# Performance work log

Measured on AMD Instinct MI355X. Metric: run time of the kernel, lower is better.

The kernel has to match this reference:

```python
import jax, jax.numpy as jnp
import numpy as np

CELU_ALPHA = 0.1  # torchani default
DIMS = [384, 160, 128, 96, 1]


def setup_inputs() -> dict:
    key = jax.random.key(0)
    ks = jax.random.split(key, 10)
    E, N, D = 4, 200000, DIMS[0]
    species = jax.random.randint(ks[0], (1, N), 0, E)
    aev = jax.random.normal(ks[1], (1, N, D), dtype=jnp.float32)
    params = {}
    for li in range(4):
        din, dout = DIMS[li], DIMS[li + 1]
        scale = 1.0 / np.sqrt(din)
        params[f"W{li+1}"] = jax.random.uniform(ks[2 + 2 * li], (E, din, dout), jnp.float32, -scale, scale)
        params[f"b{li+1}"] = jax.random.uniform(ks[3 + 2 * li], (E, dout), jnp.float32, -scale, scale)
    return dict(aev=aev, species=species, **params)


def _celu(x):
    return jax.nn.celu(x, alpha=CELU_ALPHA)


def reference(aev, species, W1, b1, W2, b2, W3, b3, W4, b4):
    # aev: [1, N, D] -> flatten(0,1) like the torch code; species: [1, N]
    x = aev.reshape(-1, aev.shape[-1])            # [N, D]
    sp = species.reshape(-1)                       # [N]
    E = W1.shape[0]
    # Run every expert MLP over all rows (jit-friendly equivalent of the
    # per-species index_select dispatch); mask-combine at the end.
    h = _celu(jnp.einsum('nd,edh->enh', x, W1) + b1[:, None, :])   # [E, N, 160]
    h = _celu(jnp.einsum('enh,ehk->enk', h, W2) + b2[:, None, :])  # [E, N, 128]
    h = _celu(jnp.einsum('enk,ekm->enm', h, W3) + b3[:, None, :])  # [E, N, 96]
    out = (jnp.einsum('enm,emo->eno', h, W4) + b4[:, None, :])[..., 0]  # [E, N]
    onehot = jax.nn.one_hot(sp, E, dtype=out.dtype)                # [N, E]
    # energy_list[i] = sum over atoms with species==i of net_i output
    energy_list = jnp.sum(out * onehot.T, axis=1)                  # [E]
    return jnp.sum(energy_list, keepdims=True)                     # [1]
```

## Files before the change

### kernel.cpp

```cpp
#include <hip/hip_runtime.h>
#include <hip/hip_bf16.h>
#include <stdint.h>

typedef __attribute__((ext_vector_type(8))) short bf16x8;
typedef __attribute__((ext_vector_type(4))) float f32x4;
#define MFMA16 __builtin_amdgcn_mfma_f32_16x16x32_bf16

__device__ __forceinline__ float celu_f(float x) {
    return x > 0.f ? x : 0.1f * (__expf(x * 10.f) - 1.f);
}
__device__ __forceinline__ uint16_t bfb(float x) {
    __hip_bfloat16 h = __float2bfloat16(x);
    return *reinterpret_cast<const uint16_t*>(&h);
}
__device__ __forceinline__ uint32_t pack2(float lo, float hi) {
    return (uint32_t)bfb(lo) | ((uint32_t)bfb(hi) << 16);
}
__device__ __forceinline__ bf16x8 cvt8(float4 a, float4 b) {
    bf16x8 r;
    r[0] = (short)bfb(a.x); r[1] = (short)bfb(a.y); r[2] = (short)bfb(a.z); r[3] = (short)bfb(a.w);
    r[4] = (short)bfb(b.x); r[5] = (short)bfb(b.y); r[6] = (short)bfb(b.z); r[7] = (short)bfb(b.w);
    return r;
}
__device__ __forceinline__ void gload16(const void* g, void* l) {
    __builtin_amdgcn_global_load_lds(
        (const __attribute__((address_space(1))) unsigned int*)g,
        (__attribute__((address_space(3))) unsigned int*)l, 16, 0, 0);
}

template <int DIN, int DOUT>
__global__ void wsplit_kernel(const float* __restrict__ W, __hip_bfloat16* __restrict__ out) {
    constexpr int MB = DOUT / 16, KB = DIN / 32;
    constexpr int PER_E = MB * KB * 512;
    const int idx = blockIdx.x * 256 + threadIdx.x;
    if (idx >= 4 * PER_E) return;
    const int e = idx / PER_E;
    int r = idx % PER_E;
    const int mb = r / (KB * 512); r %= KB * 512;
    const int kb = r / 512;        r %= 512;
    const int l = r / 8, j = r % 8;
    const int m = mb * 16 + (l % 16);
    const int k = kb * 32 + (l / 16) * 8 + j;
    const float w = W[((size_t)e * DIN + k) * DOUT + m];
    const __hip_bfloat16 hi = __float2bfloat16(w);
    const float lof = w - __bfloat162float(hi);
    const size_t base = (size_t)(idx / 8) * 16;
    out[base + j]     = hi;
    out[base + 8 + j] = __float2bfloat16(lof);
}

__global__ void bucket_kernel(const int* __restrict__ species, int N,
                              int* __restrict__ counts, int* __restrict__ bidx) {
    __shared__ int lcount[4];
    __shared__ int lbase[4];
    const int t = threadIdx.x;
    if (t < 4) lcount[t] = 0;
    __syncthreads();
    const int n = blockIdx.x * blockDim.x + t;
    int sp = 0, lo = 0;
    const bool valid = (n < N);
    if (valid) {
        sp = species[n];
        lo = atomicAdd(&lcount[sp], 1);
    }
    __syncthreads();
    if (t < 4) lbase[t] = atomicAdd(&counts[t], lcount[t]);
    __syncthreads();
    if (valid) bidx[sp * N + lbase[sp] + lo] = n;
}

__global__ void sched_kernel(const int* __restrict__ counts, int* __restrict__ tbase) {
    if (threadIdx.x == 0 && blockIdx.x == 0) {
        int tacc = 0;
        tbase[0] = 0;
        for (int e = 0; e < 4; ++e) { tacc += (counts[e] + 127) >> 7; tbase[e + 1] = tacc; }
    }
}

__device__ __forceinline__ void stage_for(int s, int e, int w, int l,
                                          const char* w1b, const char* w2b,
                                          const char* w3b, char* slot) {
    if (s >= 42) return;
    const int half = s & 1;
    if (s < 24) {
        const int kb = s >> 1;
        for (int u = w; u < 10; u += 4) {
            const int mb = half * 5 + (u >> 1), h = u & 1;
            const char* src = w1b + ((((size_t)e * 10 + mb) * 12 + kb) << 11) + l * 32 + h * 16;
            gload16(src, slot + u * 1024);
        }
    } else if (s < 34) {
        const int kb = (s - 24) >> 1;
        for (int u = w; u < 8; u += 4) {
            const int mb = half * 4 + (u >> 1), h = u & 1;
            const char* src = w2b + ((((size_t)e * 8 + mb) * 5 + kb) << 11) + l * 32 + h * 16;
            gload16(src, slot + u * 1024);
        }
    } else {
        const int kb = (s - 34) >> 1;
        for (int u = w; u < 6; u += 4) {
            const int mb = half * 3 + (u >> 1), h = u & 1;
            const char* src = w3b + ((((size_t)e * 6 + mb) * 4 + kb) << 11) + l * 32 + h * 16;
            gload16(src, slot + u * 1024);
        }
    }
}

template <int MBH>
__device__ __forceinline__ void consume_slot(const char* slot, int l,
                                             bf16x8 x0, bf16x8 x1, f32x4 (*acc)[2]) {
#pragma unroll
    for (int i = 0; i < MBH; ++i) {
        const bf16x8 whi = *(const bf16x8*)(slot + i * 2048 + l * 16);
        const bf16x8 wlo = *(const bf16x8*)(slot + i * 2048 + 1024 + l * 16);
        acc[i][0] = MFMA16(whi, x0, acc[i][0], 0, 0, 0);
        acc[i][0] = MFMA16(wlo, x0, acc[i][0], 0, 0, 0);
        acc[i][1] = MFMA16(whi, x1, acc[i][1], 0, 0, 0);
        acc[i][1] = MFMA16(wlo, x1, acc[i][1], 0, 0, 0);
    }
}

template <int MB>
__device__ __forceinline__ void pack_epi(const f32x4 (*acc)[2], const float* bb, int q,
                                         uint32_t (*pk)[2][2]) {
    const int fr = q * 4;
#pragma unroll
    for (int mb = 0; mb < MB; ++mb) {
        const float4 bl = *(const float4*)(bb + mb * 16 + fr);
        const float bv[4] = {bl.x, bl.y, bl.z, bl.w};
#pragma unroll
        for (int c = 0; c < 2; ++c) {
            const float o0 = celu_f(acc[mb][c][0] + bv[0]);
            const float o1 = celu_f(acc[mb][c][1] + bv[1]);
            const float o2 = celu_f(acc[mb][c][2] + bv[2]);
            const float o3 = celu_f(acc[mb][c][3] + bv[3]);
            pk[mb][c][0] = pack2(o0, o1);
            pk[mb][c][1] = pack2(o2, o3);
        }
    }
}

__device__ __forceinline__ bf16x8 xchg(uint32_t pe0, uint32_t pe1,
                                       uint32_t po0, uint32_t po1, int a, int q) {
    union { uint32_t u[4]; bf16x8 v; } r;
#pragma unroll
    for (int d = 0; d < 4; ++d) {
        const int src = a + 16 * ((2 * q + (d >> 1)) & 3);
        const uint32_t ve = __shfl((d & 1) ? pe1 : pe0, src);
        const uint32_t vo = __shfl((d & 1) ? po1 : po0, src);
        r.u[d] = (q >= 2) ? vo : ve;
    }
    return r.v;
}

__global__ __launch_bounds__(256, 3) void mlp_mfma_kernel(
    const float* __restrict__ aev, const int* __restrict__ bidx,
    const int* __restrict__ counts, const int* __restrict__ tbase, int N,
    const __hip_bfloat16* __restrict__ wsw1, const float* __restrict__ b1,
    const __hip_bfloat16* __restrict__ wsw2, const float* __restrict__ b2,
    const __hip_bfloat16* __restrict__ wsw3, const float* __restrict__ b3,
    const float* __restrict__ W4, const float* __restrict__ b4,
    float* __restrict__ partials) {
    __shared__ __align__(16) char Wslot[2][10240];
    const int b = blockIdx.x, t = threadIdx.x;
    const int tb1 = tbase[1], tb2 = tbase[2], tb3 = tbase[3], tb4 = tbase[4];
    if (b >= tb4) return;
    const int e = (b >= tb1) + (b >= tb2) + (b >= tb3);
    const int tile = b - (e == 0 ? 0 : e == 1 ? tb1 : e == 2 ? tb2 : tb3);
    const int cnt = counts[e];
    const int w = t >> 6, l = t & 63;
    const int wbase = tile * 128 + w * 32;
    const int a = l & 15, q = l >> 4;
    const int g0 = wbase + a, g1 = wbase + 16 + a;
    const bool v0g = g0 < cnt, v1g = g1 < cnt;
    const int i0 = bidx[e * N + min(g0, cnt - 1)];
    const int i1 = bidx[e * N + min(g1, cnt - 1)];
    const float* row0 = aev + (size_t)i0 * 384 + q * 8;
    const float* row1 = aev + (size_t)i1 * 384 + q * 8;

    const char* w1b = (const char*)wsw1;
    const char* w2b = (const char*)wsw2;
    const char* w3b = (const char*)wsw3;

    float4 na = *(const float4*)(row0);
    float4 nb = *(const float4*)(row0 + 4);
    float4 nc = *(const float4*)(row1);
    float4 nd = *(const float4*)(row1 + 4);
    stage_for(0, e, w, l, w1b, w2b, w3b, &Wslot[0][0]);
    __syncthreads();

    int step = 0;

    f32x4 acc1[10][2] = {};
#pragma unroll 1
    for (int kb = 0; kb < 12; ++kb) {
        const bf16x8 x0 = cvt8(na, nb), x1 = cvt8(nc, nd);
        stage_for(step + 1, e, w, l, w1b, w2b, w3b, &Wslot[(step + 1) & 1][0]);
        consume_slot<5>(&Wslot[step & 1][0], l, x0, x1, &acc1[0]);
        __syncthreads(); ++step;
        if (kb < 11) {
            na = *(const float4*)(row0 + (kb + 1) * 32);
            nb = *(const float4*)(row0 + (kb + 1) * 32 + 4);
            nc = *(const float4*)(row1 + (kb + 1) * 32);
            nd = *(const float4*)(row1 + (kb + 1) * 32 + 4);
        }
        stage_for(step + 1, e, w, l, w1b, w2b, w3b, &Wslot[(step + 1) & 1][0]);
        consume_slot<5>(&Wslot[step & 1][0], l, x0, x1, &acc1[5]);
        __syncthreads(); ++step;
    }

    uint32_t pk1[10][2][2];
    pack_epi<10>(acc1, b1 + e * 160, q, pk1);

    f32x4 acc2[8][2] = {};
#pragma unroll
    for (int kb2 = 0; kb2 < 5; ++kb2) {
        const bf16x8 h0 = xchg(pk1[2 * kb2][0][0], pk1[2 * kb2][0][1],
                               pk1[2 * kb2 + 1][0][0], pk1[2 * kb2 + 1][0][1], a, q);
        const bf16x8 h1 = xchg(pk1[2 * kb2][1][0], pk1[2 * kb2][1][1],
                               pk1[2 * kb2 + 1][1][0], pk1[2 * kb2 + 1][1][1], a, q);
        const int s0 = 24 + 2 * kb2;
        stage_for(s0 + 1, e, w, l, w1b, w2b, w3b, &Wslot[(s0 + 1) & 1][0]);
        consume_slot<4>(&Wslot[s0 & 1][0], l, h0, h1, &acc2[0]);
        __syncthreads();
        stage_for(s0 + 2, e, w, l, w1b, w2b, w3b, &Wslot[(s0 + 2) & 1][0]);
        consume_slot<4>(&Wslot[(s0 + 1) & 1][0], l, h0, h1, &acc2[4]);
        __syncthreads();
    }

    uint32_t pk2[8][2][2];
    pack_epi<8>(acc2, b2 + e * 128, q, pk2);

    f32x4 acc3[6][2] = {};
#pragma unroll
    for (int kb3 = 0; kb3 < 4; ++kb3) {
        const bf16x8 h0 = xchg(pk2[2 * kb3][0][0], pk2[2 * kb3][0][1],
                               pk2[2 * kb3 + 1][0][0], pk2[2 * kb3 + 1][0][1], a, q);
        const bf16x8 h1 = xchg(pk2[2 * kb3][1][0], pk2[2 * kb3][1][1],
                               pk2[2 * kb3 + 1][1][0], pk2[2 * kb3 + 1][1][1], a, q);
        const int s0 = 34 + 2 * kb3;
        stage_for(s0 + 1, e, w, l, w1b, w2b, w3b, &Wslot[(s0 + 1) & 1][0]);
        consume_slot<3>(&Wslot[s0 & 1][0], l, h0, h1, &acc3[0]);
        __syncthreads();
        stage_for(s0 + 2, e, w, l, w1b, w2b, w3b, &Wslot[(s0 + 2) & 1][0]);
        consume_slot<3>(&Wslot[(s0 + 1) & 1][0], l, h0, h1, &acc3[3]);
        __syncthreads();
    }

    const int fr = q * 4;
    float en0 = 0.f, en1 = 0.f;
#pragma unroll
    for (int mb = 0; mb < 6; ++mb) {
        const float4 bl = *(const float4*)(b3 + e * 96 + mb * 16 + fr);
        const float4 wv = *(const float4*)(W4 + e * 96 + mb * 16 + fr);
        const float bv[4] = {bl.x, bl.y, bl.z, bl.w};
        const float wb[4] = {wv.x, wv.y, wv.z, wv.w};
#pragma unroll
        for (int r = 0; r < 4; ++r) {
            en0 += celu_f(acc3[mb][0][r] + bv[r]) * wb[r];
            en1 += celu_f(acc3[mb][1][r] + bv[r]) * wb[r];
        }
    }
    en0 += __shfl_xor(en0, 16); en0 += __shfl_xor(en0, 32);
    en1 += __shfl_xor(en1, 16); en1 += __shfl_xor(en1, 32);
    const float b4e = b4[e];
    float p = 0.f;
    if (l < 16) p = (v0g ? en0 + b4e : 0.f) + (v1g ? en1 + b4e : 0.f);
#pragma unroll
    for (int off = 1; off <= 32; off <<= 1) p += __shfl_xor(p, off);
    if (l == 0) partials[b * 4 + w] = p;
}

__global__ void reduce_kernel(const float* __restrict__ partials,
                              const int* __restrict__ tbase, float* __restrict__ out) {
    __shared__ float wsum[4];
    const int n = tbase[4] * 4;
    const int t = threadIdx.x;
    float s = 0.f;
    for (int i = t; i < n; i += 256) s += partials[i];
#pragma unroll
    for (int off = 32; off; off >>= 1) s += __shfl_down(s, off);
    if ((t & 63) == 0) wsum[t >> 6] = s;
    __syncthreads();
    if (t == 0) out[0] = wsum[0] + wsum[1] + wsum[2] + wsum[3];
}

extern "C" void kernel_launch(void* const* d_in, const int* in_sizes, int n_in,
                              void* d_out, int out_size, void* d_ws, size_t ws_size,
                              hipStream_t stream) {
    const float* aev     = (const float*)d_in[0];
    const int*   species = (const int*)d_in[1];
    const float* W1 = (const float*)d_in[2];
    const float* b1 = (const float*)d_in[3];
    const float* W2 = (const float*)d_in[4];
    const float* b2 = (const float*)d_in[5];
    const float* W3 = (const float*)d_in[6];
    const float* b3 = (const float*)d_in[7];
    const float* W4 = (const float*)d_in[8];
    const float* b4 = (const float*)d_in[9];
    float* out = (float*)d_out;

    const int N = in_sizes[1];
    const int gridx_max = (N + 127) / 128 + 4;

    char* ws = (char*)d_ws;
    int* counts = (int*)ws;
    int* tbase  = (int*)(ws + 16);
    float* partials = (float*)(ws + 256);
    size_t off = 256 + (size_t)gridx_max * 4 * sizeof(float);
    off = (off + 255) & ~(size_t)255;
    __hip_bfloat16* wsw1 = (__hip_bfloat16*)(ws + off); off += (size_t)4 * 384 * 160 * 2 * 2;
    __hip_bfloat16* wsw2 = (__hip_bfloat16*)(ws + off); off += (size_t)4 * 160 * 128 * 2 * 2;
    __hip_bfloat16* wsw3 = (__hip_bfloat16*)(ws + off); off += (size_t)4 * 128 * 96 * 2 * 2;
    int* bidx = (int*)(ws + off);

    hipMemsetAsync(d_ws, 0, 16, stream);

    wsplit_kernel<384, 160><<<(4 * 384 * 160 + 255) / 256, 256, 0, stream>>>(W1, wsw1);
    wsplit_kernel<160, 128><<<(4 * 160 * 128 + 255) / 256, 256, 0, stream>>>(W2, wsw2);
    wsplit_kernel<128, 96><<<(4 * 128 * 96 + 255) / 256, 256, 0, stream>>>(W3, wsw3);

    bucket_kernel<<<(N + 255) / 256, 256, 0, stream>>>(species, N, counts, bidx);
    sched_kernel<<<1, 64, 0, stream>>>(counts, tbase);

    mlp_mfma_kernel<<<gridx_max, 256, 0, stream>>>(aev, bidx, counts, tbase, N,
                                                   wsw1, b1, wsw2, b2, wsw3, b3, W4, b4,
                                                   partials);

    reduce_kernel<<<1, 256, 0, stream>>>(partials, tbase, out);
}
```

Before: 175.6 us.

## Restructure MLP K-loop barriers to prefetch activations earlier and drop memset

Replaces __syncthreads with a custom vmcnt(0)+s_barrier placed before each stage/consume pair, so the LDS double buffer is synchronized at the top of each step rather than the end. Next-chunk activation loads are issued right after the barrier into separate registers, which gives them more time in flight. The separate hipMemsetAsync is removed and the counts buffer is zeroed inside the first wsplit kernel launch, saving one enqueue. This uses more registers for the prefetch copies and relies on the hand-placed waitcnt covering the global_load_lds traffic.

```diff
diff --git a/kernel.cpp b/kernel.cpp
--- a/kernel.cpp
+++ b/kernel.cpp
@@ -27,9 +27,16 @@
         (const __attribute__((address_space(1))) unsigned int*)g,
         (__attribute__((address_space(3))) unsigned int*)l, 16, 0, 0);
 }
+__device__ __forceinline__ void wait_barrier() {
+    asm volatile("s_waitcnt vmcnt(0)" ::: "memory");
+    asm volatile("s_barrier" ::: "memory");
+    __builtin_amdgcn_sched_barrier(0);
+}
 
 template <int DIN, int DOUT>
-__global__ void wsplit_kernel(const float* __restrict__ W, __hip_bfloat16* __restrict__ out) {
+__global__ void wsplit_kernel(const float* __restrict__ W, __hip_bfloat16* __restrict__ out,
+                              int* counts_zero) {
+    if (counts_zero && blockIdx.x == 0 && threadIdx.x < 4) counts_zero[threadIdx.x] = 0;
     constexpr int MB = DOUT / 16, KB = DIN / 32;
     constexpr int PER_E = MB * KB * 512;
     const int idx = blockIdx.x * 256 + threadIdx.x;
@@ -187,26 +194,25 @@
     float4 nc = *(const float4*)(row1);
     float4 nd = *(const float4*)(row1 + 4);
     stage_for(0, e, w, l, w1b, w2b, w3b, &Wslot[0][0]);
-    __syncthreads();
-
-    int step = 0;
 
     f32x4 acc1[10][2] = {};
+    float4 pa, pb, pc, pd;
 #pragma unroll 1
     for (int kb = 0; kb < 12; ++kb) {
+        wait_barrier();
+        if (kb < 11) {
+            pa = *(const float4*)(row0 + (kb + 1) * 32);
+            pb = *(const float4*)(row0 + (kb + 1) * 32 + 4);
+            pc = *(const float4*)(row1 + (kb + 1) * 32);
+            pd = *(const float4*)(row1 + (kb + 1) * 32 + 4);
+        }
         const bf16x8 x0 = cvt8(na, nb), x1 = cvt8(nc, nd);
-        stage_for(step + 1, e, w, l, w1b, w2b, w3b, &Wslot[(step + 1) & 1][0]);
-        consume_slot<5>(&Wslot[step & 1][0], l, x0, x1, &acc1[0]);
-        __syncthreads(); ++step;
-        if (kb < 11) {
-            na = *(const float4*)(row0 + (kb + 1) * 32);
-            nb = *(const float4*)(row0 + (kb + 1) * 32 + 4);
-            nc = *(const float4*)(row1 + (kb + 1) * 32);
-            nd = *(const float4*)(row1 + (kb + 1) * 32 + 4);
-        }
-        stage_for(step + 1, e, w, l, w1b, w2b, w3b, &Wslot[(step + 1) & 1][0]);
-        consume_slot<5>(&Wslot[step & 1][0], l, x0, x1, &acc1[5]);
-        __syncthreads(); ++step;
+        stage_for(2 * kb + 1, e, w, l, w1b, w2b, w3b, &Wslot[(2 * kb + 1) & 1][0]);
+        consume_slot<5>(&Wslot[(2 * kb) & 1][0], l, x0, x1, &acc1[0]);
+        wait_barrier();
+        stage_for(2 * kb + 2, e, w, l, w1b, w2b, w3b, &Wslot[(2 * kb + 2) & 1][0]);
+        consume_slot<5>(&Wslot[(2 * kb + 1) & 1][0], l, x0, x1, &acc1[5]);
+        na = pa; nb = pb; nc = pc; nd = pd;
     }
 
     uint32_t pk1[10][2][2];
@@ -220,12 +226,12 @@
         const bf16x8 h1 = xchg(pk1[2 * kb2][1][0], pk1[2 * kb2][1][1],
                                pk1[2 * kb2 + 1][1][0], pk1[2 * kb2 + 1][1][1], a, q);
         const int s0 = 24 + 2 * kb2;
+        wait_barrier();
         stage_for(s0 + 1, e, w, l, w1b, w2b, w3b, &Wslot[(s0 + 1) & 1][0]);
         consume_slot<4>(&Wslot[s0 & 1][0], l, h0, h1, &acc2[0]);
-        __syncthreads();
+        wait_barrier();
         stage_for(s0 + 2, e, w, l, w1b, w2b, w3b, &Wslot[(s0 + 2) & 1][0]);
         consume_slot<4>(&Wslot[(s0 + 1) & 1][0], l, h0, h1, &acc2[4]);
-        __syncthreads();
     }
 
     uint32_t pk2[8][2][2];
@@ -239,12 +245,12 @@
         const bf16x8 h1 = xchg(pk2[2 * kb3][1][0], pk2[2 * kb3][1][1],
                                pk2[2 * kb3 + 1][1][0], pk2[2 * kb3 + 1][1][1], a, q);
         const int s0 = 34 + 2 * kb3;
+        wait_barrier();
         stage_for(s0 + 1, e, w, l, w1b, w2b, w3b, &Wslot[(s0 + 1) & 1][0]);
         consume_slot<3>(&Wslot[s0 & 1][0], l, h0, h1, &acc3[0]);
-        __syncthreads();
+        wait_barrier();
         stage_for(s0 + 2, e, w, l, w1b, w2b, w3b, &Wslot[(s0 + 2) & 1][0]);
         consume_slot<3>(&Wslot[(s0 + 1) & 1][0], l, h0, h1, &acc3[3]);
-        __syncthreads();
     }
 
     const int fr = q * 4;
@@ -314,11 +320,9 @@
     __hip_bfloat16* wsw3 = (__hip_bfloat16*)(ws + off); off += (size_t)4 * 128 * 96 * 2 * 2;
     int* bidx = (int*)(ws + off);
 
-    hipMemsetAsync(d_ws, 0, 16, stream);
-
-    wsplit_kernel<384, 160><<<(4 * 384 * 160 + 255) / 256, 256, 0, stream>>>(W1, wsw1);
-    wsplit_kernel<160, 128><<<(4 * 160 * 128 + 255) / 256, 256, 0, stream>>>(W2, wsw2);
-    wsplit_kernel<128, 96><<<(4 * 128 * 96 + 255) / 256, 256, 0, stream>>>(W3, wsw3);
+    wsplit_kernel<384, 160><<<(4 * 384 * 160 + 255) / 256, 256, 0, stream>>>(W1, wsw1, counts);
+    wsplit_kernel<160, 128><<<(4 * 160 * 128 + 255) / 256, 256, 0, stream>>>(W2, wsw2, nullptr);
+    wsplit_kernel<128, 96><<<(4 * 128 * 96 + 255) / 256, 256, 0, stream>>>(W3, wsw3, nullptr);
 
     bucket_kernel<<<(N + 255) / 256, 256, 0, stream>>>(species, N, counts, bidx);
     sched_kernel<<<1, 64, 0, stream>>>(counts, tbase);
```

After: 179.7 us. 2.3% more time.
